# Performance work log

Hardware: AMD Instinct MI355X
Metric: run time of the kernel (lower is better)

## Reference

```python
import jax, jax.numpy as jnp
import numpy as np

BATCH, K, N = 16384, 512, 1024  # codewords, message_length, code_length


def setup_inputs() -> dict:
    key = jax.random.key(0)
    kx, km = jax.random.split(key)
    # binary message bits as float32 (as the torch module casts with .float())
    x = jnp.round(jax.random.uniform(kx, (BATCH, K), dtype=jnp.float32))
    # binary polar generator matrix [K, N]
    matrix = jnp.round(jax.random.uniform(km, (K, N), dtype=jnp.float32))
    return {"x": x, "matrix": matrix}


def reference(x, matrix):
    # GF(2) encoding: (x @ G) mod 2, returned as integer codeword bits
    codeword = jnp.remainder(x @ matrix, 2.0)
    return codeword.astype(jnp.int32)
```

## Files before the change

kernel.cpp:

```cpp
#include <hip/hip_runtime.h>
#include <stdint.h>

#define BATCH 16384
#define KDIM  512
#define NDIM  1024
#define NW    16
#define THREADS 256
#define ROWS_PER_BLOCK 16
#define PHASE_ROWS 2
#define NPHASE (ROWS_PER_BLOCK / PHASE_ROWS)

typedef int i32x4 __attribute__((ext_vector_type(4)));

__global__ __launch_bounds__(256) void pack_g_kernel(const float* __restrict__ G,
                                                     uint32_t* __restrict__ Gt) {
    __shared__ uint32_t nib[8][32];
    const int bid = blockIdx.x;
    const int m   = bid >> 5;
    const int n0  = (bid & 31) << 5;
    const int tid = threadIdx.x;
    const int p   = tid >> 5;
    const int nn  = tid & 31;
    const int kbase = 256 * (m >> 3) + 128 * ((m >> 2) & 1) + (m & 3);
    uint32_t w = 0;
#pragma unroll
    for (int j = 0; j < 4; ++j) {
        int c = 4 * p + j;
        w |= (uint32_t)(G[(size_t)(kbase + 4 * c) * NDIM + n0 + nn] > 0.5f) << c;
    }
    nib[p][nn] = w;
    __syncthreads();
    if (tid < 32) {
        uint32_t r = nib[0][tid] | nib[1][tid] | nib[2][tid] | nib[3][tid]
                   | nib[4][tid] | nib[5][tid] | nib[6][tid] | nib[7][tid];
        Gt[m * NDIM + n0 + tid] = r;
    }
}

__global__ __launch_bounds__(THREADS, 4)
void gf2_fused_kernel(const float* __restrict__ x,
                      const uint32_t* __restrict__ Gt,
                      int* __restrict__ out) {
    const int tid = threadIdx.x;
    const int w   = tid >> 6;
    const int l   = tid & 63;
    const int q   = w >> 1;
    const int h   = w & 1;
    const int row0 = blockIdx.x * ROWS_PER_BLOCK;

    uint32_t g0[NW], g1[NW], g2[NW], g3[NW];
#pragma unroll
    for (int m = 0; m < NW; ++m) {
        uint4 gg = reinterpret_cast<const uint4*>(Gt + m * NDIM)[tid];
        g0[m] = gg.x;
        g1[m] = gg.y;
        g2[m] = gg.z;
        g3[m] = gg.w;
    }

    __shared__ __align__(16) uint32_t xw[2][PHASE_ROWS][NW];

    const float4* xf = reinterpret_cast<const float4*>(x);
    float4 f = xf[(size_t)row0 * (KDIM / 4) + tid];

    for (int p = 0; p < NPHASE; ++p) {
        uint64_t b0 = __ballot(f.x > 0.5f);
        uint64_t b1 = __ballot(f.y > 0.5f);
        uint64_t b2 = __ballot(f.z > 0.5f);
        uint64_t b3 = __ballot(f.w > 0.5f);

        if (p + 1 < NPHASE)
            f = xf[(size_t)(row0 + (p + 1) * PHASE_ROWS) * (KDIM / 4) + tid];

        if (l == 0) {
            uint32_t* dst = &xw[p & 1][q][h * 8];
            dst[0] = (uint32_t)b0;  dst[4] = (uint32_t)(b0 >> 32);
            dst[1] = (uint32_t)b1;  dst[5] = (uint32_t)(b1 >> 32);
            dst[2] = (uint32_t)b2;  dst[6] = (uint32_t)(b2 >> 32);
            dst[3] = (uint32_t)b3;  dst[7] = (uint32_t)(b3 >> 32);
        }
        __syncthreads();

        size_t obase = (size_t)(row0 + p * PHASE_ROWS) * NDIM + 4 * (size_t)tid;
#pragma unroll
        for (int r = 0; r < PHASE_ROWS; ++r) {
            const uint4* x4 = reinterpret_cast<const uint4*>(&xw[p & 1][r][0]);
            uint4 a0 = x4[0], a1 = x4[1], a2 = x4[2], a3 = x4[3];
            uint32_t t0 = (a0.x & g0[0])  ^ (a0.y & g0[1])  ^ (a0.z & g0[2])  ^ (a0.w & g0[3])
                        ^ (a1.x & g0[4])  ^ (a1.y & g0[5])  ^ (a1.z & g0[6])  ^ (a1.w & g0[7])
                        ^ (a2.x & g0[8])  ^ (a2.y & g0[9])  ^ (a2.z & g0[10]) ^ (a2.w & g0[11])
                        ^ (a3.x & g0[12]) ^ (a3.y & g0[13]) ^ (a3.z & g0[14]) ^ (a3.w & g0[15]);
            uint32_t t1 = (a0.x & g1[0])  ^ (a0.y & g1[1])  ^ (a0.z & g1[2])  ^ (a0.w & g1[3])
                        ^ (a1.x & g1[4])  ^ (a1.y & g1[5])  ^ (a1.z & g1[6])  ^ (a1.w & g1[7])
                        ^ (a2.x & g1[8])  ^ (a2.y & g1[9])  ^ (a2.z & g1[10]) ^ (a2.w & g1[11])
                        ^ (a3.x & g1[12]) ^ (a3.y & g1[13]) ^ (a3.z & g1[14]) ^ (a3.w & g1[15]);
            uint32_t t2 = (a0.x & g2[0])  ^ (a0.y & g2[1])  ^ (a0.z & g2[2])  ^ (a0.w & g2[3])
                        ^ (a1.x & g2[4])  ^ (a1.y & g2[5])  ^ (a1.z & g2[6])  ^ (a1.w & g2[7])
                        ^ (a2.x & g2[8])  ^ (a2.y & g2[9])  ^ (a2.z & g2[10]) ^ (a2.w & g2[11])
                        ^ (a3.x & g2[12]) ^ (a3.y & g2[13]) ^ (a3.z & g2[14]) ^ (a3.w & g2[15]);
            uint32_t t3 = (a0.x & g3[0])  ^ (a0.y & g3[1])  ^ (a0.z & g3[2])  ^ (a0.w & g3[3])
                        ^ (a1.x & g3[4])  ^ (a1.y & g3[5])  ^ (a1.z & g3[6])  ^ (a1.w & g3[7])
                        ^ (a2.x & g3[8])  ^ (a2.y & g3[9])  ^ (a2.z & g3[10]) ^ (a2.w & g3[11])
                        ^ (a3.x & g3[12]) ^ (a3.y & g3[13]) ^ (a3.z & g3[14]) ^ (a3.w & g3[15]);
            i32x4 o;
            o.x = (int)(__popc(t0) & 1u);
            o.y = (int)(__popc(t1) & 1u);
            o.z = (int)(__popc(t2) & 1u);
            o.w = (int)(__popc(t3) & 1u);
            *reinterpret_cast<i32x4*>(out + obase + (size_t)r * NDIM) = o;
        }
    }
}

extern "C" void kernel_launch(void* const* d_in, const int* in_sizes, int n_in,
                              void* d_out, int out_size, void* d_ws, size_t ws_size,
                              hipStream_t stream) {
    const float* x = (const float*)d_in[0];
    const float* G = (const float*)d_in[1];
    int* out = (int*)d_out;

    uint32_t* Gt = (uint32_t*)d_ws;

    pack_g_kernel<<<512, 256, 0, stream>>>(G, Gt);
    gf2_fused_kernel<<<BATCH / ROWS_PER_BLOCK, THREADS, 0, stream>>>(x, Gt, out);
}
```

Baseline: 28.74 us.

## Have each wavefront ballot full rows itself, removing shared memory and barriers

Each wavefront now loads a full 512-element row of x (two float4 per lane) and ballots it itself, so the bit masks sit in uniform registers and no shared-memory exchange or __syncthreads is needed. Wavefronts now split output columns instead of sharing row packing. The cost is that every wavefront loads and ballots every row, four times the x load and ballot work per block, in exchange for removing the per-phase block barrier and LDS round trip.

Measured after the change: 29.45 us. 2.5% more time.

```diff
diff --git a/kernel.cpp b/kernel.cpp
--- a/kernel.cpp
+++ b/kernel.cpp
@@ -7,8 +7,6 @@
 #define NW    16
 #define THREADS 256
 #define ROWS_PER_BLOCK 16
-#define PHASE_ROWS 2
-#define NPHASE (ROWS_PER_BLOCK / PHASE_ROWS)
 
 typedef int i32x4 __attribute__((ext_vector_type(4)));
 
@@ -44,71 +42,72 @@
     const int tid = threadIdx.x;
     const int w   = tid >> 6;
     const int l   = tid & 63;
-    const int q   = w >> 1;
-    const int h   = w & 1;
     const int row0 = blockIdx.x * ROWS_PER_BLOCK;
+    const int colbase = w * 256 + 4 * l;
 
     uint32_t g0[NW], g1[NW], g2[NW], g3[NW];
 #pragma unroll
     for (int m = 0; m < NW; ++m) {
-        uint4 gg = reinterpret_cast<const uint4*>(Gt + m * NDIM)[tid];
+        uint4 gg = *reinterpret_cast<const uint4*>(Gt + m * NDIM + colbase);
         g0[m] = gg.x;
         g1[m] = gg.y;
         g2[m] = gg.z;
         g3[m] = gg.w;
     }
 
-    __shared__ __align__(16) uint32_t xw[2][PHASE_ROWS][NW];
+    const float4* xf = reinterpret_cast<const float4*>(x);
 
-    const float4* xf = reinterpret_cast<const float4*>(x);
-    float4 f = xf[(size_t)row0 * (KDIM / 4) + tid];
+    float4 fA = xf[(size_t)row0 * (KDIM / 4) + l];
+    float4 fB = xf[(size_t)row0 * (KDIM / 4) + 64 + l];
 
-    for (int p = 0; p < NPHASE; ++p) {
-        uint64_t b0 = __ballot(f.x > 0.5f);
-        uint64_t b1 = __ballot(f.y > 0.5f);
-        uint64_t b2 = __ballot(f.z > 0.5f);
-        uint64_t b3 = __ballot(f.w > 0.5f);
+#pragma unroll 2
+    for (int r = 0; r < ROWS_PER_BLOCK; ++r) {
+        uint64_t bA0 = __ballot(fA.x > 0.5f);
+        uint64_t bA1 = __ballot(fA.y > 0.5f);
+        uint64_t bA2 = __ballot(fA.z > 0.5f);
+        uint64_t bA3 = __ballot(fA.w > 0.5f);
+        uint64_t bB0 = __ballot(fB.x > 0.5f);
+        uint64_t bB1 = __ballot(fB.y > 0.5f);
+        uint64_t bB2 = __ballot(fB.z > 0.5f);
+        uint64_t bB3 = __ballot(fB.w > 0.5f);
 
-        if (p + 1 < NPHASE)
-            f = xf[(size_t)(row0 + (p + 1) * PHASE_ROWS) * (KDIM / 4) + tid];
+        if (r + 1 < ROWS_PER_BLOCK) {
+            fA = xf[(size_t)(row0 + r + 1) * (KDIM / 4) + l];
+            fB = xf[(size_t)(row0 + r + 1) * (KDIM / 4) + 64 + l];
+        }
 
-        if (l == 0) {
-            uint32_t* dst = &xw[p & 1][q][h * 8];
-            dst[0] = (uint32_t)b0;  dst[4] = (uint32_t)(b0 >> 32);
-            dst[1] = (uint32_t)b1;  dst[5] = (uint32_t)(b1 >> 32);
-            dst[2] = (uint32_t)b2;  dst[6] = (uint32_t)(b2 >> 32);
-            dst[3] = (uint32_t)b3;  dst[7] = (uint32_t)(b3 >> 32);
-        }
-        __syncthreads();
+        uint32_t m0  = (uint32_t)bA0,  m1  = (uint32_t)bA1;
+        uint32_t m2  = (uint32_t)bA2,  m3  = (uint32_t)bA3;
+        uint32_t m4  = (uint32_t)(bA0 >> 32), m5  = (uint32_t)(bA1 >> 32);
+        uint32_t m6  = (uint32_t)(bA2 >> 32), m7  = (uint32_t)(bA3 >> 32);
+        uint32_t m8  = (uint32_t)bB0,  m9  = (uint32_t)bB1;
+        uint32_t m10 = (uint32_t)bB2,  m11 = (uint32_t)bB3;
+        uint32_t m12 = (uint32_t)(bB0 >> 32), m13 = (uint32_t)(bB1 >> 32);
+        uint32_t m14 = (uint32_t)(bB2 >> 32), m15 = (uint32_t)(bB3 >> 32);
 
-        size_t obase = (size_t)(row0 + p * PHASE_ROWS) * NDIM + 4 * (size_t)tid;
-#pragma unroll
-        for (int r = 0; r < PHASE_ROWS; ++r) {
-            const uint4* x4 = reinterpret_cast<const uint4*>(&xw[p & 1][r][0]);
-            uint4 a0 = x4[0], a1 = x4[1], a2 = x4[2], a3 = x4[3];
-            uint32_t t0 = (a0.x & g0[0])  ^ (a0.y & g0[1])  ^ (a0.z & g0[2])  ^ (a0.w & g0[3])
-                        ^ (a1.x & g0[4])  ^ (a1.y & g0[5])  ^ (a1.z & g0[6])  ^ (a1.w & g0[7])
-                        ^ (a2.x & g0[8])  ^ (a2.y & g0[9])  ^ (a2.z & g0[10]) ^ (a2.w & g0[11])
-                        ^ (a3.x & g0[12]) ^ (a3.y & g0[13]) ^ (a3.z & g0[14]) ^ (a3.w & g0[15]);
-            uint32_t t1 = (a0.x & g1[0])  ^ (a0.y & g1[1])  ^ (a0.z & g1[2])  ^ (a0.w & g1[3])
-                        ^ (a1.x & g1[4])  ^ (a1.y & g1[5])  ^ (a1.z & g1[6])  ^ (a1.w & g1[7])
-                        ^ (a2.x & g1[8])  ^ (a2.y & g1[9])  ^ (a2.z & g1[10]) ^ (a2.w & g1[11])
-                        ^ (a3.x & g1[12]) ^ (a3.y & g1[13]) ^ (a3.z & g1[14]) ^ (a3.w & g1[15]);
-            uint32_t t2 = (a0.x & g2[0])  ^ (a0.y & g2[1])  ^ (a0.z & g2[2])  ^ (a0.w & g2[3])
-                        ^ (a1.x & g2[4])  ^ (a1.y & g2[5])  ^ (a1.z & g2[6])  ^ (a1.w & g2[7])
-                        ^ (a2.x & g2[8])  ^ (a2.y & g2[9])  ^ (a2.z & g2[10]) ^ (a2.w & g2[11])
-                        ^ (a3.x & g2[12]) ^ (a3.y & g2[13]) ^ (a3.z & g2[14]) ^ (a3.w & g2[15]);
-            uint32_t t3 = (a0.x & g3[0])  ^ (a0.y & g3[1])  ^ (a0.z & g3[2])  ^ (a0.w & g3[3])
-                        ^ (a1.x & g3[4])  ^ (a1.y & g3[5])  ^ (a1.z & g3[6])  ^ (a1.w & g3[7])
-                        ^ (a2.x & g3[8])  ^ (a2.y & g3[9])  ^ (a2.z & g3[10]) ^ (a2.w & g3[11])
-                        ^ (a3.x & g3[12]) ^ (a3.y & g3[13]) ^ (a3.z & g3[14]) ^ (a3.w & g3[15]);
-            i32x4 o;
-            o.x = (int)(__popc(t0) & 1u);
-            o.y = (int)(__popc(t1) & 1u);
-            o.z = (int)(__popc(t2) & 1u);
-            o.w = (int)(__popc(t3) & 1u);
-            *reinterpret_cast<i32x4*>(out + obase + (size_t)r * NDIM) = o;
-        }
+        uint32_t t0 = (m0 & g0[0])   ^ (m1 & g0[1])   ^ (m2 & g0[2])   ^ (m3 & g0[3])
+                    ^ (m4 & g0[4])   ^ (m5 & g0[5])   ^ (m6 & g0[6])   ^ (m7 & g0[7])
+                    ^ (m8 & g0[8])   ^ (m9 & g0[9])   ^ (m10 & g0[10]) ^ (m11 & g0[11])
+                    ^ (m12 & g0[12]) ^ (m13 & g0[13]) ^ (m14 & g0[14]) ^ (m15 & g0[15]);
+        uint32_t t1 = (m0 & g1[0])   ^ (m1 & g1[1])   ^ (m2 & g1[2])   ^ (m3 & g1[3])
+                    ^ (m4 & g1[4])   ^ (m5 & g1[5])   ^ (m6 & g1[6])   ^ (m7 & g1[7])
+                    ^ (m8 & g1[8])   ^ (m9 & g1[9])   ^ (m10 & g1[10]) ^ (m11 & g1[11])
+                    ^ (m12 & g1[12]) ^ (m13 & g1[13]) ^ (m14 & g1[14]) ^ (m15 & g1[15]);
+        uint32_t t2 = (m0 & g2[0])   ^ (m1 & g2[1])   ^ (m2 & g2[2])   ^ (m3 & g2[3])
+                    ^ (m4 & g2[4])   ^ (m5 & g2[5])   ^ (m6 & g2[6])   ^ (m7 & g2[7])
+                    ^ (m8 & g2[8])   ^ (m9 & g2[9])   ^ (m10 & g2[10]) ^ (m11 & g2[11])
+                    ^ (m12 & g2[12]) ^ (m13 & g2[13]) ^ (m14 & g2[14]) ^ (m15 & g2[15]);
+        uint32_t t3 = (m0 & g3[0])   ^ (m1 & g3[1])   ^ (m2 & g3[2])   ^ (m3 & g3[3])
+                    ^ (m4 & g3[4])   ^ (m5 & g3[5])   ^ (m6 & g3[6])   ^ (m7 & g3[7])
+                    ^ (m8 & g3[8])   ^ (m9 & g3[9])   ^ (m10 & g3[10]) ^ (m11 & g3[11])
+                    ^ (m12 & g3[12]) ^ (m13 & g3[13]) ^ (m14 & g3[14]) ^ (m15 & g3[15]);
+
+        i32x4 o;
+        o.x = (int)(__popc(t0) & 1u);
+        o.y = (int)(__popc(t1) & 1u);
+        o.z = (int)(__popc(t2) & 1u);
+        o.w = (int)(__popc(t3) & 1u);
+        *reinterpret_cast<i32x4*>(out + (size_t)(row0 + r) * NDIM + colbase) = o;
     }
 }
 
```
